# Optimization experiments

Measured on AMD Instinct MI355X. Metric: run time of the kernel, lower is better.

The kernel has to match this reference:

```python
import jax, jax.numpy as jnp
import numpy as np

N = 100000      # nodes
E = 1600000     # edges (avg degree 16)
F_IN = 128
HID = 128
LAT = 64


def gat_conv(x, src, dst, W, a_src, a_dst, b, n):
    """PyG GATConv (single aggregation): lin -> per-edge LeakyReLU(0.2) attention
    -> segment softmax over incoming edges of each dst node -> weighted scatter-add -> bias.
    W: [F_in, H*C], a_src/a_dst: [H, C], b: [H*C] (concat) or [C] (H=1 either way)."""
    H, C = a_src.shape
    h = (x @ W).reshape(n, H, C)                              # [N,H,C]
    al_s = jnp.einsum('nhc,hc->nh', h, a_src)                 # [N,H]
    al_d = jnp.einsum('nhc,hc->nh', h, a_dst)                 # [N,H]
    e = jax.nn.leaky_relu(al_s[src] + al_d[dst], 0.2)         # [E,H]
    emax = jax.lax.stop_gradient(jax.ops.segment_max(e, dst, num_segments=n))
    ee = jnp.exp(e - emax[dst])                               # stable segment softmax
    den = jax.ops.segment_sum(ee, dst, num_segments=n)
    alpha = ee / (den[dst] + 1e-16)                           # [E,H]
    out = jax.ops.segment_sum(h[src] * alpha[:, :, None], dst, num_segments=n)  # [N,H,C]
    return out.reshape(n, H * C) + b


def setup_inputs() -> dict:
    key = jax.random.key(0)
    ks = jax.random.split(key, 24)
    s = 0.05
    inp = {
        'x': jax.random.normal(ks[0], (N, F_IN), jnp.float32),
        'edge_index': jax.random.randint(ks[1], (2, E), 0, N, jnp.int64),
        # layer 0 GATConv (in -> hid, H=1) + self linear
        'W0': jax.random.normal(ks[2], (F_IN, HID), jnp.float32) * s,
        'a_src0': jax.random.normal(ks[3], (1, HID), jnp.float32) * s,
        'a_dst0': jax.random.normal(ks[4], (1, HID), jnp.float32) * s,
        'b0': jnp.zeros((HID,), jnp.float32),
        'slW0': jax.random.normal(ks[5], (F_IN, HID), jnp.float32) * s,
        'slb0': jnp.zeros((HID,), jnp.float32),
        # layer 1 GATConv (hid -> hid, H=1) + self linear
        'W1': jax.random.normal(ks[6], (HID, HID), jnp.float32) * s,
        'a_src1': jax.random.normal(ks[7], (1, HID), jnp.float32) * s,
        'a_dst1': jax.random.normal(ks[8], (1, HID), jnp.float32) * s,
        'b1': jnp.zeros((HID,), jnp.float32),
        'slW1': jax.random.normal(ks[9], (HID, HID), jnp.float32) * s,
        'slb1': jnp.zeros((HID,), jnp.float32),
        # mu / logvar heads (hid -> lat, H=1, concat=False)
        'Wmu': jax.random.normal(ks[10], (HID, LAT), jnp.float32) * s,
        'a_src_mu': jax.random.normal(ks[11], (1, LAT), jnp.float32) * s,
        'a_dst_mu': jax.random.normal(ks[12], (1, LAT), jnp.float32) * s,
        'b_mu': jnp.zeros((LAT,), jnp.float32),
        'Wlv': jax.random.normal(ks[13], (HID, LAT), jnp.float32) * s,
        'a_src_lv': jax.random.normal(ks[14], (1, LAT), jnp.float32) * s,
        'a_dst_lv': jax.random.normal(ks[15], (1, LAT), jnp.float32) * s,
        'b_lv': jnp.zeros((LAT,), jnp.float32),
    }
    return inp


def reference(x, edge_index, W0, a_src0, a_dst0, b0, slW0, slb0,
              W1, a_src1, a_dst1, b1, slW1, slb1,
              Wmu, a_src_mu, a_dst_mu, b_mu, Wlv, a_src_lv, a_dst_lv, b_lv):
    src, dst = edge_index[0], edge_index[1]
    loop = jnp.arange(N, dtype=edge_index.dtype)
    src_sl = jnp.concatenate([src, loop])   # layers with add_self_loops=True
    dst_sl = jnp.concatenate([dst, loop])
    # layer 0: GATConv(add_self_loops=False) + Linear, then LeakyReLU(0.01)
    h = gat_conv(x, src, dst, W0, a_src0, a_dst0, b0, N) + x @ slW0 + slb0
    h = jax.nn.leaky_relu(h, 0.01)
    # layer 1: GATConv(default self loops) + Linear, then LeakyReLU(0.01)
    h = gat_conv(h, src_sl, dst_sl, W1, a_src1, a_dst1, b1, N) + h @ slW1 + slb1
    h = jax.nn.leaky_relu(h, 0.01)
    mu = gat_conv(h, src_sl, dst_sl, Wmu, a_src_mu, a_dst_mu, b_mu, N)
    logvar = gat_conv(h, src_sl, dst_sl, Wlv, a_src_lv, a_dst_lv, b_lv, N)
    return (mu, logvar)
```

## Files before the change

kernel.cpp:

```cpp
#include <hip/hip_runtime.h>
#include <cstdint>
#include <cstddef>

__device__ __forceinline__ float bf2f(unsigned short u) {
  return __uint_as_float(((unsigned)u) << 16);
}
__device__ __forceinline__ unsigned short f2bf(float f) {
  unsigned u = __float_as_uint(f);
  u = (u + 0x7FFFu + ((u >> 16) & 1u)) >> 16;
  return (unsigned short)u;
}

typedef __attribute__((ext_vector_type(8))) short bf16x8;
typedef __attribute__((ext_vector_type(4))) float f32x4;

__global__ void detect_kernel(const int* __restrict__ ei, int* __restrict__ flag) {
  int any = 0;
  for (int j = threadIdx.x; j < 4096; j += 256) any |= (ei[2 * j + 1] != 0);
  if (any) atomicOr(flag, 1);
}

__device__ __forceinline__ int edge_src(const int* ei, int f, int e, int i) {
  return f ? ei[i] : ei[2 * (size_t)i];
}
__device__ __forceinline__ int edge_dst(const int* ei, int f, int e, int i) {
  return f ? ei[(size_t)e + i] : ei[2 * (size_t)e + 2 * (size_t)i];
}

__global__ void hist_kernel(const int* __restrict__ ei, const int* __restrict__ flag,
                            int* __restrict__ cnt, int e) {
  int i = blockIdx.x * blockDim.x + threadIdx.x;
  if (i < e) atomicAdd(&cnt[edge_dst(ei, *flag, e, i)], 1);
}

__global__ void scan_block(const int* __restrict__ cnt, int* __restrict__ rp,
                           int* __restrict__ bsum, int n) {
  __shared__ int lds[256];
  const int t = threadIdx.x;
  const int base = blockIdx.x * 1024 + t * 4;
  int v0 = (base     < n) ? cnt[base]     : 0;
  int v1 = (base + 1 < n) ? cnt[base + 1] : 0;
  int v2 = (base + 2 < n) ? cnt[base + 2] : 0;
  int v3 = (base + 3 < n) ? cnt[base + 3] : 0;
  int s = v0 + v1 + v2 + v3;
  lds[t] = s;
  __syncthreads();
  for (int off = 1; off < 256; off <<= 1) {
    int y = (t >= off) ? lds[t - off] : 0;
    __syncthreads();
    lds[t] += y;
    __syncthreads();
  }
  int excl = lds[t] - s;
  if (base     < n) rp[base]     = excl;
  if (base + 1 < n) rp[base + 1] = excl + v0;
  if (base + 2 < n) rp[base + 2] = excl + v0 + v1;
  if (base + 3 < n) rp[base + 3] = excl + v0 + v1 + v2;
  if (t == 255) bsum[blockIdx.x] = lds[255];
}

__global__ void scan_tops(int* __restrict__ bsum, int* __restrict__ rp, int nb, int n) {
  __shared__ int lds[128];
  const int t = threadIdx.x;
  int v = (t < nb) ? bsum[t] : 0;
  lds[t] = v;
  __syncthreads();
  for (int off = 1; off < 128; off <<= 1) {
    int y = (t >= off) ? lds[t - off] : 0;
    __syncthreads();
    lds[t] += y;
    __syncthreads();
  }
  if (t < nb) bsum[t] = lds[t] - v;
  if (t == 127) rp[n] = lds[127];
}

__global__ void scan_add(int* __restrict__ rp, const int* __restrict__ bsum, int n) {
  const int base = blockIdx.x * 1024 + threadIdx.x * 4;
  const int add = bsum[blockIdx.x];
#pragma unroll
  for (int i = 0; i < 4; ++i)
    if (base + i < n) rp[base + i] += add;
}

#define NB 128

__global__ void bucket_hist(const int* __restrict__ ei, const int* __restrict__ flag,
                            int* __restrict__ bhist, int e, int W) {
  __shared__ int lh[NB];
  const int t = threadIdx.x;
  if (t < NB) lh[t] = 0;
  __syncthreads();
  const int base = blockIdx.x * 4096;
  const int f = *flag;
  for (int j = t; j < 4096; j += 256) {
    int i = base + j;
    if (i < e) atomicAdd(&lh[edge_dst(ei, f, e, i) / W], 1);
  }
  __syncthreads();
  if (t < NB && lh[t]) atomicAdd(&bhist[t], lh[t]);
}

__global__ void bucket_scan(const int* __restrict__ bhist, int* __restrict__ boffs,
                            int* __restrict__ bcur) {
  __shared__ int lds[NB];
  const int t = threadIdx.x;
  int v = bhist[t];
  lds[t] = v;
  __syncthreads();
  for (int off = 1; off < NB; off <<= 1) {
    int y = (t >= off) ? lds[t - off] : 0;
    __syncthreads();
    lds[t] += y;
    __syncthreads();
  }
  int excl = lds[t] - v;
  boffs[t] = excl;
  bcur[t] = excl;
  if (t == NB - 1) boffs[NB] = lds[NB - 1];
}

__global__ void bucket_scatter(const int* __restrict__ ei, const int* __restrict__ flag,
                               int* __restrict__ bcur, int2* __restrict__ ebuf,
                               int e, int W) {
  __shared__ int lh[NB];
  __shared__ int lbase[NB];
  const int t = threadIdx.x;
  if (t < NB) lh[t] = 0;
  __syncthreads();
  const int base = blockIdx.x * 4096;
  const int f = *flag;
  for (int j = t; j < 4096; j += 256) {
    int i = base + j;
    if (i < e) atomicAdd(&lh[edge_dst(ei, f, e, i) / W], 1);
  }
  __syncthreads();
  if (t < NB) {
    lbase[t] = lh[t] ? atomicAdd(&bcur[t], lh[t]) : 0;
    lh[t] = 0;
  }
  __syncthreads();
  for (int j = t; j < 4096; j += 256) {
    int i = base + j;
    if (i < e) {
      int d = edge_dst(ei, f, e, i);
      int s = edge_src(ei, f, e, i);
      int b = d / W;
      int off = atomicAdd(&lh[b], 1);
      ebuf[lbase[b] + off] = make_int2(s, d);
    }
  }
}

__global__ void bucket_fill(const int2* __restrict__ ebuf, const int* __restrict__ boffs,
                            const int* __restrict__ rp, int* __restrict__ col,
                            int n, int W) {
  __shared__ int cur[1024];
  const int b = blockIdx.x;
  const int lo = b * W;
  const int nn = min(W, n - lo);
  if (nn <= 0) return;
  for (int i = threadIdx.x; i < nn; i += 256) cur[i] = rp[lo + i];
  __syncthreads();
  const int beg = boffs[b], end = boffs[b + 1];
  for (int p = beg + threadIdx.x; p < end; p += 256) {
    int2 sd = ebuf[p];
    int pos = atomicAdd(&cur[sd.y - lo], 1);
    col[pos] = sd.x;
  }
}

__global__ void pack_mfma_b(const float* __restrict__ Wf, unsigned short* __restrict__ Wpk) {
  int i = blockIdx.x * 256 + threadIdx.x;
  if (i >= 2048) return;
  int lane = i & 63, nt = (i >> 6) & 7, ks = i >> 9;
  int nn = lane & 15, q = lane >> 4;
  int k0 = ks * 32 + q * 8, col = nt * 16 + nn;
  unsigned short o[8];
#pragma unroll
  for (int j = 0; j < 8; ++j) o[j] = f2bf(Wf[(size_t)(k0 + j) * 128 + col]);
  uint4 u;
  u.x = (unsigned)o[0] | ((unsigned)o[1] << 16);
  u.y = (unsigned)o[2] | ((unsigned)o[3] << 16);
  u.z = (unsigned)o[4] | ((unsigned)o[5] << 16);
  u.w = (unsigned)o[6] | ((unsigned)o[7] << 16);
  *(uint4*)(Wpk + (size_t)i * 8) = u;
}

__global__ void pack_mfma_head(const float* __restrict__ Wmu, const float* __restrict__ Wlv,
                               unsigned short* __restrict__ Wpk) {
  int i = blockIdx.x * 256 + threadIdx.x;
  if (i >= 2048) return;
  int lane = i & 63, nt = (i >> 6) & 7, ks = i >> 9;
  int nn = lane & 15, q = lane >> 4;
  int k0 = ks * 32 + q * 8, col = nt * 16 + nn;
  unsigned short o[8];
#pragma unroll
  for (int j = 0; j < 8; ++j) {
    float v = (col < 64) ? Wmu[(size_t)(k0 + j) * 64 + col]
                         : Wlv[(size_t)(k0 + j) * 64 + (col - 64)];
    o[j] = f2bf(v);
  }
  uint4 u;
  u.x = (unsigned)o[0] | ((unsigned)o[1] << 16);
  u.y = (unsigned)o[2] | ((unsigned)o[3] << 16);
  u.z = (unsigned)o[4] | ((unsigned)o[5] << 16);
  u.w = (unsigned)o[6] | ((unsigned)o[7] << 16);
  *(uint4*)(Wpk + (size_t)i * 8) = u;
}

template <bool HEAD>
__launch_bounds__(256)
__global__ void gemm_mfma(const float* __restrict__ X, const unsigned short* __restrict__ Wpk,
                          const float* __restrict__ a0s, const float* __restrict__ a0d,
                          const float* __restrict__ a1s, const float* __restrict__ a1d,
                          unsigned short* __restrict__ hg,
                          float* __restrict__ als, float* __restrict__ ald, int n) {
  const int wave = threadIdx.x >> 6;
  const int lane = threadIdx.x & 63;
  const int nidx = lane & 15, q = lane >> 4;
  const int r0 = blockIdx.x * 64 + wave * 16;
  const int arow = r0 + nidx;

  f32x4 acc[8];
#pragma unroll
  for (int nt = 0; nt < 8; ++nt) acc[nt] = (f32x4){0.f, 0.f, 0.f, 0.f};

#pragma unroll
  for (int ks = 0; ks < 4; ++ks) {
    union { unsigned short u[8]; bf16x8 v; } af;
    if (arow < n) {
      const float* xp = X + (size_t)arow * 128 + ks * 32 + q * 8;
      float4 a = *(const float4*)xp;
      float4 b = *(const float4*)(xp + 4);
      af.u[0] = f2bf(a.x); af.u[1] = f2bf(a.y); af.u[2] = f2bf(a.z); af.u[3] = f2bf(a.w);
      af.u[4] = f2bf(b.x); af.u[5] = f2bf(b.y); af.u[6] = f2bf(b.z); af.u[7] = f2bf(b.w);
    } else {
#pragma unroll
      for (int j = 0; j < 8; ++j) af.u[j] = 0;
    }
    const unsigned short* bp = Wpk + ((size_t)ks * 8 * 64 + lane) * 8;
#pragma unroll
    for (int nt = 0; nt < 8; ++nt) {
      bf16x8 bfm = *(const bf16x8*)(bp + (size_t)nt * 64 * 8);
      acc[nt] = __builtin_amdgcn_mfma_f32_16x16x32_bf16(af.v, bfm, acc[nt], 0, 0, 0);
    }
  }

  float dv[8][4];
#pragma unroll
  for (int nt = 0; nt < 8; ++nt) {
#pragma unroll
    for (int r = 0; r < 4; ++r) {
      unsigned short rb = f2bf(acc[nt][r]);
      dv[nt][r] = bf2f(rb);
      int row = r0 + q * 4 + r;
      if (row < n) hg[(size_t)row * 128 + nt * 16 + nidx] = rb;
    }
  }

  if constexpr (!HEAD) {
    float ps[4] = {0, 0, 0, 0}, pd[4] = {0, 0, 0, 0};
#pragma unroll
    for (int nt = 0; nt < 8; ++nt) {
      float as_ = a0s[nt * 16 + nidx];
      float ad_ = a0d[nt * 16 + nidx];
#pragma unroll
      for (int r = 0; r < 4; ++r) {
        ps[r] = fmaf(dv[nt][r], as_, ps[r]);
        pd[r] = fmaf(dv[nt][r], ad_, pd[r]);
      }
    }
#pragma unroll
    for (int r = 0; r < 4; ++r) {
#pragma unroll
      for (int o = 8; o > 0; o >>= 1) {
        ps[r] += __shfl_xor(ps[r], o, 64);
        pd[r] += __shfl_xor(pd[r], o, 64);
      }
      int row = r0 + q * 4 + r;
      if (nidx == 0 && row < n) { als[row] = ps[r]; ald[row] = pd[r]; }
    }
  } else {
    float pms[4] = {0, 0, 0, 0}, pmd[4] = {0, 0, 0, 0};
    float pls[4] = {0, 0, 0, 0}, pld[4] = {0, 0, 0, 0};
#pragma unroll
    for (int nt = 0; nt < 4; ++nt) {
      float as_ = a0s[nt * 16 + nidx];
      float ad_ = a0d[nt * 16 + nidx];
#pragma unroll
      for (int r = 0; r < 4; ++r) {
        pms[r] = fmaf(dv[nt][r], as_, pms[r]);
        pmd[r] = fmaf(dv[nt][r], ad_, pmd[r]);
      }
    }
#pragma unroll
    for (int nt = 4; nt < 8; ++nt) {
      float as_ = a1s[(nt - 4) * 16 + nidx];
      float ad_ = a1d[(nt - 4) * 16 + nidx];
#pragma unroll
      for (int r = 0; r < 4; ++r) {
        pls[r] = fmaf(dv[nt][r], as_, pls[r]);
        pld[r] = fmaf(dv[nt][r], ad_, pld[r]);
      }
    }
#pragma unroll
    for (int r = 0; r < 4; ++r) {
#pragma unroll
      for (int o = 8; o > 0; o >>= 1) {
        pms[r] += __shfl_xor(pms[r], o, 64);
        pmd[r] += __shfl_xor(pmd[r], o, 64);
        pls[r] += __shfl_xor(pls[r], o, 64);
        pld[r] += __shfl_xor(pld[r], o, 64);
      }
      int row = r0 + q * 4 + r;
      if (nidx == 0 && row < n) {
        ((float2*)als)[row] = make_float2(pms[r], pls[r]);
        ((float2*)ald)[row] = make_float2(pmd[r], pld[r]);
      }
    }
  }
}

template <int C, bool YBF>
__launch_bounds__(256)
__global__ void gemm_k128(const float* Xv, const float* __restrict__ Wf,
                          const float* __restrict__ biasf, void* Yv, int n) {
  constexpr int TC = C / 32;
  __shared__ float xs[64 * 32];
  __shared__ float wsm[32 * C];
  const int t = threadIdx.x;
  const int tc = t & 31;
  const int trg = t >> 5;
  const int row0 = blockIdx.x * 64;

  float acc[8][TC];
#pragma unroll
  for (int i = 0; i < 8; ++i)
#pragma unroll
    for (int c = 0; c < TC; ++c) acc[i][c] = 0.f;

  for (int kc = 0; kc < 128; kc += 32) {
    {
      const int r = t >> 2;
      const int j = (t & 3) * 8;
      const int row = row0 + r;
      float v[8];
      if (row < n) {
        const float* xp = Xv + (size_t)row * 128 + kc + j;
        float4 a = *(const float4*)xp;
        float4 b = *(const float4*)(xp + 4);
        v[0] = a.x; v[1] = a.y; v[2] = a.z; v[3] = a.w;
        v[4] = b.x; v[5] = b.y; v[6] = b.z; v[7] = b.w;
      } else {
#pragma unroll
        for (int q = 0; q < 8; ++q) v[q] = 0.f;
      }
      *(float4*)&xs[r * 32 + j]     = make_float4(v[0], v[1], v[2], v[3]);
      *(float4*)&xs[r * 32 + j + 4] = make_float4(v[4], v[5], v[6], v[7]);
    }
    {
      constexpr int per = (32 * C) / 256;
      const float* wp = Wf + (size_t)kc * C + t * per;
      float* wl = wsm + t * per;
#pragma unroll
      for (int q = 0; q < per; q += 4) *(float4*)(wl + q) = *(const float4*)(wp + q);
    }
    __syncthreads();
#pragma unroll
    for (int k = 0; k < 32; k += 4) {
      float wv[4][TC];
#pragma unroll
      for (int k2 = 0; k2 < 4; ++k2) {
        if constexpr (TC == 4) {
          float4 w4 = *(const float4*)&wsm[(k + k2) * C + tc * 4];
          wv[k2][0] = w4.x; wv[k2][1] = w4.y; wv[k2][2] = w4.z; wv[k2][3] = w4.w;
        } else {
          float2 w2 = *(const float2*)&wsm[(k + k2) * C + tc * 2];
          wv[k2][0] = w2.x; wv[k2][1] = w2.y;
        }
      }
#pragma unroll
      for (int i = 0; i < 8; ++i) {
        float4 x4 = *(const float4*)&xs[(trg * 8 + i) * 32 + k];
        float xa[4] = {x4.x, x4.y, x4.z, x4.w};
#pragma unroll
        for (int k2 = 0; k2 < 4; ++k2)
#pragma unroll
          for (int c = 0; c < TC; ++c)
            acc[i][c] = fmaf(xa[k2], wv[k2][c], acc[i][c]);
      }
    }
    __syncthreads();
  }
  float bv[TC];
#pragma unroll
  for (int c = 0; c < TC; ++c) bv[c] = biasf ? biasf[tc * TC + c] : 0.f;
#pragma unroll
  for (int i = 0; i < 8; ++i) {
    const int row = row0 + trg * 8 + i;
    if (row < n) {
      float r[TC];
#pragma unroll
      for (int c = 0; c < TC; ++c) r[c] = acc[i][c] + bv[c];
      if constexpr (YBF) {
        unsigned short* yp = (unsigned short*)Yv + (size_t)row * C + tc * TC;
        if constexpr (TC == 4) {
          uint2 u;
          u.x = (unsigned)f2bf(r[0]) | ((unsigned)f2bf(r[1]) << 16);
          u.y = (unsigned)f2bf(r[2]) | ((unsigned)f2bf(r[3]) << 16);
          *(uint2*)yp = u;
        } else {
          *(unsigned*)yp = (unsigned)f2bf(r[0]) | ((unsigned)f2bf(r[1]) << 16);
        }
      } else {
        float* yp = (float*)Yv + (size_t)row * C + tc * TC;
        if constexpr (TC == 4) *(float4*)yp = make_float4(r[0], r[1], r[2], r[3]);
        else                   *(float2*)yp = make_float2(r[0], r[1]);
      }
    }
  }
}

__launch_bounds__(256)
__global__ void gat_agg3(const unsigned short* __restrict__ hg,
                         const float* __restrict__ als, const float* __restrict__ aldv,
                         const int* __restrict__ rp, const int* __restrict__ col,
                         const float* __restrict__ biasf, float* __restrict__ outv,
                         const float* base, int n, int self_loop, int act) {
  const int node = blockIdx.x * 4 + (threadIdx.x >> 6);
  if (node >= n) return;
  const int lane = threadIdx.x & 63;
  const int beg = rp[node];
  const int deg = rp[node + 1] - beg;
  const int total = deg + self_loop;
  const float ad = aldv[node];

  float m = -INFINITY, den = 0.f, a0 = 0.f, a1 = 0.f;

  for (int cb = 0; cb < total; cb += 64) {
    const int idx = cb + lane;
    const bool valid = idx < total;
    int s = node;
    if (valid && idx < deg) s = col[beg + idx];
    float l = -INFINITY;
    if (valid) {
      float v = als[s] + ad;
      l = (v > 0.f) ? v : 0.2f * v;
    }
    float cm = l;
#pragma unroll
    for (int o = 32; o > 0; o >>= 1) cm = fmaxf(cm, __shfl_xor(cm, o, 64));
    const float newm = fmaxf(m, cm);
    const float scale = __expf(m - newm);
    den *= scale; a0 *= scale; a1 *= scale;
    m = newm;
    const float e = valid ? __expf(l - m) : 0.f;
    float cd = e;
#pragma unroll
    for (int o = 32; o > 0; o >>= 1) cd += __shfl_xor(cd, o, 64);
    den += cd;

    const int cnt = (total - cb < 64) ? (total - cb) : 64;
    int j = 0;
    for (; j + 8 <= cnt; j += 8) {
      float w[8]; int ss[8]; unsigned rr[8];
#pragma unroll
      for (int u = 0; u < 8; ++u) { w[u] = __shfl(e, j + u, 64); ss[u] = __shfl(s, j + u, 64); }
#pragma unroll
      for (int u = 0; u < 8; ++u) rr[u] = *(const unsigned*)(hg + (size_t)ss[u] * 128 + 2 * lane);
#pragma unroll
      for (int u = 0; u < 8; ++u) {
        a0 = fmaf(w[u], __uint_as_float(rr[u] << 16), a0);
        a1 = fmaf(w[u], __uint_as_float(rr[u] & 0xFFFF0000u), a1);
      }
    }
    for (; j + 4 <= cnt; j += 4) {
      float w[4]; int ss[4]; unsigned rr[4];
#pragma unroll
      for (int u = 0; u < 4; ++u) { w[u] = __shfl(e, j + u, 64); ss[u] = __shfl(s, j + u, 64); }
#pragma unroll
      for (int u = 0; u < 4; ++u) rr[u] = *(const unsigned*)(hg + (size_t)ss[u] * 128 + 2 * lane);
#pragma unroll
      for (int u = 0; u < 4; ++u) {
        a0 = fmaf(w[u], __uint_as_float(rr[u] << 16), a0);
        a1 = fmaf(w[u], __uint_as_float(rr[u] & 0xFFFF0000u), a1);
      }
    }
    for (; j < cnt; ++j) {
      float wj = __shfl(e, j, 64);
      int sj = __shfl(s, j, 64);
      unsigned raw = *(const unsigned*)(hg + (size_t)sj * 128 + 2 * lane);
      a0 = fmaf(wj, __uint_as_float(raw << 16), a0);
      a1 = fmaf(wj, __uint_as_float(raw & 0xFFFF0000u), a1);
    }
  }

  const float inv = 1.f / (den + 1e-16f);
  const size_t o = (size_t)node * 128 + 2 * lane;
  float2 bv = *(const float2*)(biasf + 2 * lane);
  float r0 = a0 * inv + bv.x;
  float r1 = a1 * inv + bv.y;
  if (base) { float2 bs = *(const float2*)(base + o); r0 += bs.x; r1 += bs.y; }
  if (act) {
    r0 = (r0 > 0.f) ? r0 : 0.01f * r0;
    r1 = (r1 > 0.f) ? r1 : 0.01f * r1;
  }
  *(float2*)(outv + o) = make_float2(r0, r1);
}

__launch_bounds__(256)
__global__ void gat_agg_dual(const unsigned short* __restrict__ hg,
                             const float2* __restrict__ alsH, const float2* __restrict__ aldH,
                             const int* __restrict__ rp, const int* __restrict__ col,
                             const float* __restrict__ bmu, const float* __restrict__ blv,
                             float* __restrict__ outF, int n) {
  const int node = blockIdx.x * 4 + (threadIdx.x >> 6);
  if (node >= n) return;
  const int lane = threadIdx.x & 63;
  const bool isMu = lane < 32;
  const int beg = rp[node];
  const int deg = rp[node + 1] - beg;
  const int total = deg + 1;
  const float2 ad = aldH[node];

  float mM = -INFINITY, mL = -INFINITY, dM = 0.f, dL = 0.f;
  float a0 = 0.f, a1 = 0.f;

  for (int cb = 0; cb < total; cb += 64) {
    const int idx = cb + lane;
    const bool valid = idx < total;
    int s = node;
    if (valid && idx < deg) s = col[beg + idx];
    float lm = -INFINITY, ll = -INFINITY;
    if (valid) {
      float2 as_ = alsH[s];
      float vm = as_.x + ad.x; lm = (vm > 0.f) ? vm : 0.2f * vm;
      float vl = as_.y + ad.y; ll = (vl > 0.f) ? vl : 0.2f * vl;
    }
    float cm = lm, cl = ll;
#pragma unroll
    for (int o = 32; o > 0; o >>= 1) {
      cm = fmaxf(cm, __shfl_xor(cm, o, 64));
      cl = fmaxf(cl, __shfl_xor(cl, o, 64));
    }
    const float nM = fmaxf(mM, cm), nL = fmaxf(mL, cl);
    const float sM = __expf(mM - nM), sL = __expf(mL - nL);
    dM *= sM; dL *= sL;
    const float sc = isMu ? sM : sL;
    a0 *= sc; a1 *= sc;
    mM = nM; mL = nL;
    const float eM = valid ? __expf(lm - mM) : 0.f;
    const float eL = valid ? __expf(ll - mL) : 0.f;
    float cdM = eM, cdL = eL;
#pragma unroll
    for (int o = 32; o > 0; o >>= 1) {
      cdM += __shfl_xor(cdM, o, 64);
      cdL += __shfl_xor(cdL, o, 64);
    }
    dM += cdM; dL += cdL;

    const int cnt = (total - cb < 64) ? (total - cb) : 64;
    int j = 0;
    for (; j + 4 <= cnt; j += 4) {
      float w[4]; int ss[4]; unsigned rr[4];
#pragma unroll
      for (int u = 0; u < 4; ++u) {
        float wm = __shfl(eM, j + u, 64), wl = __shfl(eL, j + u, 64);
        w[u] = isMu ? wm : wl;
        ss[u] = __shfl(s, j + u, 64);
      }
#pragma unroll
      for (int u = 0; u < 4; ++u) rr[u] = *(const unsigned*)(hg + (size_t)ss[u] * 128 + 2 * lane);
#pragma unroll
      for (int u = 0; u < 4; ++u) {
        a0 = fmaf(w[u], __uint_as_float(rr[u] << 16), a0);
        a1 = fmaf(w[u], __uint_as_float(rr[u] & 0xFFFF0000u), a1);
      }
    }
    for (; j < cnt; ++j) {
      float wm = __shfl(eM, j, 64), wl = __shfl(eL, j, 64);
      float wj = isMu ? wm : wl;
      int sj = __shfl(s, j, 64);
      unsigned raw = *(const unsigned*)(hg + (size_t)sj * 128 + 2 * lane);
      a0 = fmaf(wj, __uint_as_float(raw << 16), a0);
      a1 = fmaf(wj, __uint_as_float(raw & 0xFFFF0000u), a1);
    }
  }

  const float inv = 1.f / ((isMu ? dM : dL) + 1e-16f);
  const int c = isMu ? 2 * lane : 2 * (lane - 32);
  const float* bb = isMu ? bmu : blv;
  float r0 = a0 * inv + bb[c];
  float r1 = a1 * inv + bb[c + 1];
  float* op = outF + (isMu ? 0 : (size_t)n * 64) + (size_t)node * 64 + c;
  *(float2*)op = make_float2(r0, r1);
}

extern "C" void kernel_launch(void* const* d_in, const int* in_sizes, int n_in,
                              void* d_out, int out_size, void* d_ws, size_t ws_size,
                              hipStream_t stream) {
  const int N = in_sizes[0] / 128;
  const int E = in_sizes[1] / 2;
  const int W = (N + NB - 1) / NB;

  const float* x    = (const float*)d_in[0];
  const int*   ei   = (const int*)d_in[1];
  const float* W0   = (const float*)d_in[2];
  const float* as0  = (const float*)d_in[3];
  const float* ad0  = (const float*)d_in[4];
  const float* b0   = (const float*)d_in[5];
  const float* slW0 = (const float*)d_in[6];
  const float* slb0 = (const float*)d_in[7];
  const float* W1   = (const float*)d_in[8];
  const float* as1  = (const float*)d_in[9];
  const float* ad1  = (const float*)d_in[10];
  const float* b1   = (const float*)d_in[11];
  const float* slW1 = (const float*)d_in[12];
  const float* slb1 = (const float*)d_in[13];
  const float* Wmu  = (const float*)d_in[14];
  const float* asmu = (const float*)d_in[15];
  const float* admu = (const float*)d_in[16];
  const float* bmu  = (const float*)d_in[17];
  const float* Wlv  = (const float*)d_in[18];
  const float* aslv = (const float*)d_in[19];
  const float* adlv = (const float*)d_in[20];
  const float* blv  = (const float*)d_in[21];

  float*          outF = (float*)d_out;
  unsigned short* hgB  = (unsigned short*)d_out;

  char* w = (char*)d_ws;
  auto carve = [&](size_t bytes) -> char* {
    char* p = w;
    w += (bytes + 255) & ~(size_t)255;
    return p;
  };
  float*          h0    = (float*)carve((size_t)N * 128 * 4);
  unsigned short* hgHd  = (unsigned short*)carve((size_t)N * 128 * 2);
  float*          als   = (float*)carve((size_t)N * 4);
  float*          ald   = (float*)carve((size_t)N * 4);
  float2*         alsH  = (float2*)carve((size_t)N * 8);
  float2*         aldH  = (float2*)carve((size_t)N * 8);
  int*            cnt   = (int*)carve((size_t)N * 4);
  int*            rp    = (int*)carve((size_t)(N + 1) * 4);
  int*            col   = (int*)carve((size_t)E * 4);
  int*            bsum  = (int*)carve(512);
  int*            bhist = (int*)carve(NB * 4);
  int*            boffs = (int*)carve((NB + 1) * 4);
  int*            bcur  = (int*)carve(NB * 4);
  int*            flag  = (int*)carve(4);
  unsigned short* Wpk0  = (unsigned short*)carve(2048 * 8 * 2);
  unsigned short* Wpk1  = (unsigned short*)carve(2048 * 8 * 2);
  unsigned short* Wpkh  = (unsigned short*)carve(2048 * 8 * 2);
  int2*           ebuf  = (int2*)h0;

  const int gE  = (E + 255) / 256;
  const int gB4 = (E + 4095) / 4096;
  const int gG  = (N + 63) / 64;
  const int gW  = (N + 3) / 4;
  const int nb  = (N + 1023) / 1024;

  hipMemsetAsync(flag, 0, 4, stream);
  hipMemsetAsync(cnt, 0, (size_t)N * 4, stream);
  hipMemsetAsync(bhist, 0, NB * 4, stream);
  detect_kernel<<<1, 256, 0, stream>>>(ei, flag);
  hist_kernel<<<gE, 256, 0, stream>>>(ei, flag, cnt, E);
  bucket_hist<<<gB4, 256, 0, stream>>>(ei, flag, bhist, E, W);
  scan_block<<<nb, 256, 0, stream>>>(cnt, rp, bsum, N);
  scan_tops<<<1, 128, 0, stream>>>(bsum, rp, nb, N);
  scan_add<<<nb, 256, 0, stream>>>(rp, bsum, N);
  bucket_scan<<<1, NB, 0, stream>>>(bhist, boffs, bcur);
  bucket_scatter<<<gB4, 256, 0, stream>>>(ei, flag, bcur, ebuf, E, W);
  bucket_fill<<<NB, 256, 0, stream>>>(ebuf, boffs, rp, col, N, W);

  pack_mfma_b<<<8, 256, 0, stream>>>(W0, Wpk0);
  pack_mfma_b<<<8, 256, 0, stream>>>(W1, Wpk1);
  pack_mfma_head<<<8, 256, 0, stream>>>(Wmu, Wlv, Wpkh);

  gemm_mfma<false><<<gG, 256, 0, stream>>>(x, Wpk0, as0, ad0, nullptr, nullptr,
                                           hgB, als, ald, N);
  gemm_k128<128, false><<<gG, 256, 0, stream>>>(x, slW0, slb0, h0, N);
  gat_agg3<<<gW, 256, 0, stream>>>(hgB, als, ald, rp, col, b0, h0, h0, N, 0, 1);

  gemm_mfma<false><<<gG, 256, 0, stream>>>(h0, Wpk1, as1, ad1, nullptr, nullptr,
                                           hgB, als, ald, N);
  gemm_k128<128, false><<<gG, 256, 0, stream>>>(h0, slW1, slb1, h0, N);
  gat_agg3<<<gW, 256, 0, stream>>>(hgB, als, ald, rp, col, b1, h0, h0, N, 1, 1);

  gemm_mfma<true><<<gG, 256, 0, stream>>>(h0, Wpkh, asmu, admu, aslv, adlv,
                                          hgHd, (float*)alsH, (float*)aldH, N);
  gat_agg_dual<<<gW, 256, 0, stream>>>(hgHd, alsH, aldH, rp, col, bmu, blv, outF, N);
}
```

Baseline: 693.2 us.

## Use 16-lane groups per node with vectorized gathers and drop online softmax max

Assigns 16 lanes per destination node instead of a full 64-lane wave, so each lane gathers 8 bf16 features with one 16-byte load. Removes the running max and its wave-wide reductions: unnormalized exp weights and the denominator are accumulated per lane. This targets lane underuse at low average degree and the shuffle and exp overhead. The trade-off is that exp without max subtraction can overflow for large attention logits.

```diff
diff --git a/kernel.cpp b/kernel.cpp
--- a/kernel.cpp
+++ b/kernel.cpp
@@ -428,85 +428,91 @@
                          const int* __restrict__ rp, const int* __restrict__ col,
                          const float* __restrict__ biasf, float* __restrict__ outv,
                          const float* base, int n, int self_loop, int act) {
-  const int node = blockIdx.x * 4 + (threadIdx.x >> 6);
+  const int node = blockIdx.x * 16 + (threadIdx.x >> 4);
   if (node >= n) return;
-  const int lane = threadIdx.x & 63;
+  const int g = threadIdx.x & 15;
   const int beg = rp[node];
   const int deg = rp[node + 1] - beg;
   const int total = deg + self_loop;
   const float ad = aldv[node];
 
-  float m = -INFINITY, den = 0.f, a0 = 0.f, a1 = 0.f;
-
-  for (int cb = 0; cb < total; cb += 64) {
-    const int idx = cb + lane;
+  float den = 0.f;
+  float acc[8];
+#pragma unroll
+  for (int k = 0; k < 8; ++k) acc[k] = 0.f;
+
+  const unsigned short* hgl = hg + g * 8;
+
+  for (int cb = 0; cb < total; cb += 16) {
+    const int idx = cb + g;
     const bool valid = idx < total;
     int s = node;
     if (valid && idx < deg) s = col[beg + idx];
-    float l = -INFINITY;
+    float e = 0.f;
     if (valid) {
       float v = als[s] + ad;
-      l = (v > 0.f) ? v : 0.2f * v;
-    }
-    float cm = l;
-#pragma unroll
-    for (int o = 32; o > 0; o >>= 1) cm = fmaxf(cm, __shfl_xor(cm, o, 64));
-    const float newm = fmaxf(m, cm);
-    const float scale = __expf(m - newm);
-    den *= scale; a0 *= scale; a1 *= scale;
-    m = newm;
-    const float e = valid ? __expf(l - m) : 0.f;
-    float cd = e;
-#pragma unroll
-    for (int o = 32; o > 0; o >>= 1) cd += __shfl_xor(cd, o, 64);
-    den += cd;
-
-    const int cnt = (total - cb < 64) ? (total - cb) : 64;
+      float l = (v > 0.f) ? v : 0.2f * v;
+      e = __expf(l);
+    }
+
+    const int cnt = (total - cb < 16) ? (total - cb) : 16;
     int j = 0;
-    for (; j + 8 <= cnt; j += 8) {
-      float w[8]; int ss[8]; unsigned rr[8];
-#pragma unroll
-      for (int u = 0; u < 8; ++u) { w[u] = __shfl(e, j + u, 64); ss[u] = __shfl(s, j + u, 64); }
-#pragma unroll
-      for (int u = 0; u < 8; ++u) rr[u] = *(const unsigned*)(hg + (size_t)ss[u] * 128 + 2 * lane);
-#pragma unroll
-      for (int u = 0; u < 8; ++u) {
-        a0 = fmaf(w[u], __uint_as_float(rr[u] << 16), a0);
-        a1 = fmaf(w[u], __uint_as_float(rr[u] & 0xFFFF0000u), a1);
-      }
-    }
     for (; j + 4 <= cnt; j += 4) {
-      float w[4]; int ss[4]; unsigned rr[4];
-#pragma unroll
-      for (int u = 0; u < 4; ++u) { w[u] = __shfl(e, j + u, 64); ss[u] = __shfl(s, j + u, 64); }
-#pragma unroll
-      for (int u = 0; u < 4; ++u) rr[u] = *(const unsigned*)(hg + (size_t)ss[u] * 128 + 2 * lane);
+      float w[4]; int ss[4]; uint4 rr[4];
+#pragma unroll
+      for (int u = 0; u < 4; ++u) { w[u] = __shfl(e, j + u, 16); ss[u] = __shfl(s, j + u, 16); }
+#pragma unroll
+      for (int u = 0; u < 4; ++u) rr[u] = *(const uint4*)(hgl + (size_t)ss[u] * 128);
 #pragma unroll
       for (int u = 0; u < 4; ++u) {
-        a0 = fmaf(w[u], __uint_as_float(rr[u] << 16), a0);
-        a1 = fmaf(w[u], __uint_as_float(rr[u] & 0xFFFF0000u), a1);
+        den += w[u];
+        acc[0] = fmaf(w[u], __uint_as_float(rr[u].x << 16),        acc[0]);
+        acc[1] = fmaf(w[u], __uint_as_float(rr[u].x & 0xFFFF0000u), acc[1]);
+        acc[2] = fmaf(w[u], __uint_as_float(rr[u].y << 16),        acc[2]);
+        acc[3] = fmaf(w[u], __uint_as_float(rr[u].y & 0xFFFF0000u), acc[3]);
+        acc[4] = fmaf(w[u], __uint_as_float(rr[u].z << 16),        acc[4]);
+        acc[5] = fmaf(w[u], __uint_as_float(rr[u].z & 0xFFFF0000u), acc[5]);
+        acc[6] = fmaf(w[u], __uint_as_float(rr[u].w << 16),        acc[6]);
+        acc[7] = fmaf(w[u], __uint_as_float(rr[u].w & 0xFFFF0000u), acc[7]);
       }
     }
     for (; j < cnt; ++j) {
-      float wj = __shfl(e, j, 64);
-      int sj = __shfl(s, j, 64);
-      unsigned raw = *(const unsigned*)(hg + (size_t)sj * 128 + 2 * lane);
-      a0 = fmaf(wj, __uint_as_float(raw << 16), a0);
-      a1 = fmaf(wj, __uint_as_float(raw & 0xFFFF0000u), a1);
+      float wj = __shfl(e, j, 16);
+      int sj = __shfl(s, j, 16);
+      uint4 raw = *(const uint4*)(hgl + (size_t)sj * 128);
+      den += wj;
+      acc[0] = fmaf(wj, __uint_as_float(raw.x << 16),        acc[0]);
+      acc[1] = fmaf(wj, __uint_as_float(raw.x & 0xFFFF0000u), acc[1]);
+      acc[2] = fmaf(wj, __uint_as_float(raw.y << 16),        acc[2]);
+      acc[3] = fmaf(wj, __uint_as_float(raw.y & 0xFFFF0000u), acc[3]);
+      acc[4] = fmaf(wj, __uint_as_float(raw.z << 16),        acc[4]);
+      acc[5] = fmaf(wj, __uint_as_float(raw.z & 0xFFFF0000u), acc[5]);
+      acc[6] = fmaf(wj, __uint_as_float(raw.w << 16),        acc[6]);
+      acc[7] = fmaf(wj, __uint_as_float(raw.w & 0xFFFF0000u), acc[7]);
     }
   }
 
   const float inv = 1.f / (den + 1e-16f);
-  const size_t o = (size_t)node * 128 + 2 * lane;
-  float2 bv = *(const float2*)(biasf + 2 * lane);
-  float r0 = a0 * inv + bv.x;
-  float r1 = a1 * inv + bv.y;
-  if (base) { float2 bs = *(const float2*)(base + o); r0 += bs.x; r1 += bs.y; }
+  const size_t o = (size_t)node * 128 + g * 8;
+  float4 bv0 = *(const float4*)(biasf + g * 8);
+  float4 bv1 = *(const float4*)(biasf + g * 8 + 4);
+  float r[8];
+  r[0] = acc[0] * inv + bv0.x; r[1] = acc[1] * inv + bv0.y;
+  r[2] = acc[2] * inv + bv0.z; r[3] = acc[3] * inv + bv0.w;
+  r[4] = acc[4] * inv + bv1.x; r[5] = acc[5] * inv + bv1.y;
+  r[6] = acc[6] * inv + bv1.z; r[7] = acc[7] * inv + bv1.w;
+  if (base) {
+    float4 s0 = *(const float4*)(base + o);
+    float4 s1 = *(const float4*)(base + o + 4);
+    r[0] += s0.x; r[1] += s0.y; r[2] += s0.z; r[3] += s0.w;
+    r[4] += s1.x; r[5] += s1.y; r[6] += s1.z; r[7] += s1.w;
+  }
   if (act) {
-    r0 = (r0 > 0.f) ? r0 : 0.01f * r0;
-    r1 = (r1 > 0.f) ? r1 : 0.01f * r1;
-  }
-  *(float2*)(outv + o) = make_float2(r0, r1);
+#pragma unroll
+    for (int k = 0; k < 8; ++k) r[k] = (r[k] > 0.f) ? r[k] : 0.01f * r[k];
+  }
+  *(float4*)(outv + o)     = make_float4(r[0], r[1], r[2], r[3]);
+  *(float4*)(outv + o + 4) = make_float4(r[4], r[5], r[6], r[7]);
 }
 
 __launch_bounds__(256)
@@ -515,86 +521,88 @@
                              const int* __restrict__ rp, const int* __restrict__ col,
                              const float* __restrict__ bmu, const float* __restrict__ blv,
                              float* __restrict__ outF, int n) {
-  const int node = blockIdx.x * 4 + (threadIdx.x >> 6);
+  const int node = blockIdx.x * 16 + (threadIdx.x >> 4);
   if (node >= n) return;
-  const int lane = threadIdx.x & 63;
-  const bool isMu = lane < 32;
+  const int g = threadIdx.x & 15;
+  const bool isMu = g < 8;
   const int beg = rp[node];
   const int deg = rp[node + 1] - beg;
   const int total = deg + 1;
   const float2 ad = aldH[node];
 
-  float mM = -INFINITY, mL = -INFINITY, dM = 0.f, dL = 0.f;
-  float a0 = 0.f, a1 = 0.f;
-
-  for (int cb = 0; cb < total; cb += 64) {
-    const int idx = cb + lane;
+  float den = 0.f;
+  float acc[8];
+#pragma unroll
+  for (int k = 0; k < 8; ++k) acc[k] = 0.f;
+
+  const unsigned short* hgl = hg + g * 8;
+
+  for (int cb = 0; cb < total; cb += 16) {
+    const int idx = cb + g;
     const bool valid = idx < total;
     int s = node;
     if (valid && idx < deg) s = col[beg + idx];
-    float lm = -INFINITY, ll = -INFINITY;
+    float eM = 0.f, eL = 0.f;
     if (valid) {
       float2 as_ = alsH[s];
-      float vm = as_.x + ad.x; lm = (vm > 0.f) ? vm : 0.2f * vm;
-      float vl = as_.y + ad.y; ll = (vl > 0.f) ? vl : 0.2f * vl;
-    }
-    float cm = lm, cl = ll;
-#pragma unroll
-    for (int o = 32; o > 0; o >>= 1) {
-      cm = fmaxf(cm, __shfl_xor(cm, o, 64));
-      cl = fmaxf(cl, __shfl_xor(cl, o, 64));
-    }
-    const float nM = fmaxf(mM, cm), nL = fmaxf(mL, cl);
-    const float sM = __expf(mM - nM), sL = __expf(mL - nL);
-    dM *= sM; dL *= sL;
-    const float sc = isMu ? sM : sL;
-    a0 *= sc; a1 *= sc;
-    mM = nM; mL = nL;
-    const float eM = valid ? __expf(lm - mM) : 0.f;
-    const float eL = valid ? __expf(ll - mL) : 0.f;
-    float cdM = eM, cdL = eL;
-#pragma unroll
-    for (int o = 32; o > 0; o >>= 1) {
-      cdM += __shfl_xor(cdM, o, 64);
-      cdL += __shfl_xor(cdL, o, 64);
-    }
-    dM += cdM; dL += cdL;
-
-    const int cnt = (total - cb < 64) ? (total - cb) : 64;
+      float vm = as_.x + ad.x;
+      float vl = as_.y + ad.y;
+      eM = __expf((vm > 0.f) ? vm : 0.2f * vm);
+      eL = __expf((vl > 0.f) ? vl : 0.2f * vl);
+    }
+
+    const int cnt = (total - cb < 16) ? (total - cb) : 16;
     int j = 0;
     for (; j + 4 <= cnt; j += 4) {
-      float w[4]; int ss[4]; unsigned rr[4];
+      float w[4]; int ss[4]; uint4 rr[4];
 #pragma unroll
       for (int u = 0; u < 4; ++u) {
-        float wm = __shfl(eM, j + u, 64), wl = __shfl(eL, j + u, 64);
+        float wm = __shfl(eM, j + u, 16), wl = __shfl(eL, j + u, 16);
         w[u] = isMu ? wm : wl;
-        ss[u] = __shfl(s, j + u, 64);
-      }
-#pragma unroll
-      for (int u = 0; u < 4; ++u) rr[u] = *(const unsigned*)(hg + (size_t)ss[u] * 128 + 2 * lane);
+        ss[u] = __shfl(s, j + u, 16);
+      }
+#pragma unroll
+      for (int u = 0; u < 4; ++u) rr[u] = *(const uint4*)(hgl + (size_t)ss[u] * 128);
 #pragma unroll
       for (int u = 0; u < 4; ++u) {
-        a0 = fmaf(w[u], __uint_as_float(rr[u] << 16), a0);
-        a1 = fmaf(w[u], __uint_as_float(rr[u] & 0xFFFF0000u), a1);
+        den += w[u];
+        acc[0] = fmaf(w[u], __uint_as_float(rr[u].x << 16),        acc[0]);
+        acc[1] = fmaf(w[u], __uint_as_float(rr[u].x & 0xFFFF0000u), acc[1]);
+        acc[2] = fmaf(w[u], __uint_as_float(rr[u].y << 16),        acc[2]);
+        acc[3] = fmaf(w[u], __uint_as_float(rr[u].y & 0xFFFF0000u), acc[3]);
+        acc[4] = fmaf(w[u], __uint_as_float(rr[u].z << 16),        acc[4]);
+        acc[5] = fmaf(w[u], __uint_as_float(rr[u].z & 0xFFFF0000u), acc[5]);
+        acc[6] = fmaf(w[u], __uint_as_float(rr[u].w << 16),        acc[6]);
+        acc[7] = fmaf(w[u], __uint_as_float(rr[u].w & 0xFFFF0000u), acc[7]);
       }
     }
     for (; j < cnt; ++j) {
-      float wm = __shfl(eM, j, 64), wl = __shfl(eL, j, 64);
+      float wm = __shfl(eM, j, 16), wl = __shfl(eL, j, 16);
       float wj = isMu ? wm : wl;
-      int sj = __shfl(s, j, 64);
-      unsigned raw = *(const unsigned*)(hg + (size_t)sj * 128 + 2 * lane);
-      a0 = fmaf(wj, __uint_as_float(raw << 16), a0);
-      a1 = fmaf(wj, __uint_as_float(raw & 0xFFFF0000u), a1);
-    }
-  }
-
-  const float inv = 1.f / ((isMu ? dM : dL) + 1e-16f);
-  const int c = isMu ? 2 * lane : 2 * (lane - 32);
+      int sj = __shfl(s, j, 16);
+      uint4 raw = *(const uint4*)(hgl + (size_t)sj * 128);
+      den += wj;
+      acc[0] = fmaf(wj, __uint_as_float(raw.x << 16),        acc[0]);
+      acc[1] = fmaf(wj, __uint_as_float(raw.x & 0xFFFF0000u), acc[1]);
+      acc[2] = fmaf(wj, __uint_as_float(raw.y << 16),        acc[2]);
+      acc[3] = fmaf(wj, __uint_as_float(raw.y & 0xFFFF0000u), acc[3]);
+      acc[4] = fmaf(wj, __uint_as_float(raw.z << 16),        acc[4]);
+      acc[5] = fmaf(wj, __uint_as_float(raw.z & 0xFFFF0000u), acc[5]);
+      acc[6] = fmaf(wj, __uint_as_float(raw.w << 16),        acc[6]);
+      acc[7] = fmaf(wj, __uint_as_float(raw.w & 0xFFFF0000u), acc[7]);
+    }
+  }
+
+  const float inv = 1.f / (den + 1e-16f);
+  const int c = (g & 7) * 8;
   const float* bb = isMu ? bmu : blv;
-  float r0 = a0 * inv + bb[c];
-  float r1 = a1 * inv + bb[c + 1];
-  float* op = outF + (isMu ? 0 : (size_t)n * 64) + (size_t)node * 64 + c;
-  *(float2*)op = make_float2(r0, r1);
+  float4 bv0 = *(const float4*)(bb + c);
+  float4 bv1 = *(const float4*)(bb + c + 4);
+  float* op = outF + (isMu ? (size_t)0 : (size_t)n * 64) + (size_t)node * 64 + c;
+  *(float4*)op = make_float4(acc[0] * inv + bv0.x, acc[1] * inv + bv0.y,
+                             acc[2] * inv + bv0.z, acc[3] * inv + bv0.w);
+  *(float4*)(op + 4) = make_float4(acc[4] * inv + bv1.x, acc[5] * inv + bv1.y,
+                                   acc[6] * inv + bv1.z, acc[7] * inv + bv1.w);
 }
 
 extern "C" void kernel_launch(void* const* d_in, const int* in_sizes, int n_in,
@@ -658,7 +666,7 @@
   const int gE  = (E + 255) / 256;
   const int gB4 = (E + 4095) / 4096;
   const int gG  = (N + 63) / 64;
-  const int gW  = (N + 3) / 4;
+  const int gW  = (N + 15) / 16;
   const int nb  = (N + 1023) / 1024;
 
   hipMemsetAsync(flag, 0, 4, stream);
```

Result: faster. 671.3 us (-3.2%).
